# Optimization experiments

Hardware: AMD Instinct MI355X
Metric: run time of the kernel (lower is better)

The kernel has to match this reference:

```python
import jax, jax.numpy as jnp
import numpy as np

K = 10          # top-k history news selected per candidate
THRESHOLD = 0.1 # attention-weight threshold (config.threshold)
EPS = 1e-12     # F.normalize eps


def setup_inputs() -> dict:
    key = jax.random.key(0)
    k1, k2, k3, k4 = jax.random.split(key, 4)
    B, C, H, L, LEV, D = 32, 5, 50, 32, 3, 256
    return {
        "cdd_repr": jax.random.normal(k1, (B, C, D), dtype=jnp.float32),
        "his_repr": jax.random.normal(k2, (B, H, D), dtype=jnp.float32),
        "his_embedding": jax.random.normal(k3, (B, H, L, LEV, D), dtype=jnp.float32),
        "W_sel": jax.random.normal(k4, (D, D), dtype=jnp.float32) * (1.0 / np.sqrt(D)),
        "b_sel": jnp.zeros((D,), dtype=jnp.float32),
    }


def _l2norm(x):
    # F.normalize(x, dim=-1): x / max(||x||, eps)
    n = jnp.sqrt(jnp.sum(x * x, axis=-1, keepdims=True))
    return x / jnp.maximum(n, EPS)


def reference(cdd_repr, his_repr, his_embedding, W_sel, b_sel):
    # selectionProject (Linear) + L2 normalize
    c = _l2norm(cdd_repr @ W_sel + b_sel)      # [B, C, D]
    h = _l2norm(his_repr @ W_sel + b_sel)      # [B, H, D]
    # news-level attention scores: cdd x his
    attn = jnp.einsum('bcd,bhd->bch', c, h)    # [B, C, H]
    # top-k over history
    w, idx = jax.lax.top_k(attn, K)            # [B, C, K]
    # gather selected history embeddings: [B, C, K, L, LEV, D]
    B = his_embedding.shape[0]
    his_activated = his_embedding[jnp.arange(B)[:, None, None], idx]
    # threshold masking then scale activated embeddings by attention weight
    w_masked = jnp.where(w < THRESHOLD, 0.0, w)
    his_activated = his_activated * w_masked[:, :, :, None, None, None]
    return his_activated
```

## Files before the change

kernel.cpp:

```cpp
#include <hip/hip_runtime.h>
#include <math.h>

#define BB 32
#define CC 5
#define HH 50
#define LL 32
#define LEV 3
#define DD 256
#define KK 10
#define THRESH 0.1f
#define EPSF 1e-12f
#define RPB 8
#define NPROJ ((BB * CC + BB * HH) / RPB)
#define INNER (LL * LEV * DD)
#define INNER4 (INNER / 4)
#define NBCK (BB * CC * KK)
#define CHUNKS 4
#define PERCH (INNER4 / CHUNKS)

typedef float f32x4 __attribute__((ext_vector_type(4)));

__device__ __forceinline__ void store_stream(f32x4 v, f32x4* p) {
    asm volatile("global_store_dwordx4 %0, %1, off sc0 sc1 nt"
                 :: "v"(p), "v"(v) : "memory");
}

__global__ void proj_norm_kernel(const float* __restrict__ cdd,
                                 const float* __restrict__ his,
                                 const float* __restrict__ W,
                                 const float* __restrict__ bias,
                                 float* __restrict__ c_out,
                                 float* __restrict__ h_out)
{
    const int row0 = blockIdx.x * RPB;
    const int j    = threadIdx.x;
    const int wid  = j >> 6;
    const int lane = j & 63;

    __shared__ float xs[RPB][DD];
    #pragma unroll
    for (int r = 0; r < RPB; ++r) {
        const int row = row0 + r;
        const float* x = (row < BB * CC) ? (cdd + (size_t)row * DD)
                                         : (his + (size_t)(row - BB * CC) * DD);
        xs[r][j] = x[j];
    }
    __syncthreads();

    const float bj = bias[j];
    float acc[RPB];
    #pragma unroll
    for (int r = 0; r < RPB; ++r) acc[r] = bj;

    for (int d = 0; d < DD; d += 4) {
        const float w0 = W[(size_t)(d + 0) * DD + j];
        const float w1 = W[(size_t)(d + 1) * DD + j];
        const float w2 = W[(size_t)(d + 2) * DD + j];
        const float w3 = W[(size_t)(d + 3) * DD + j];
        #pragma unroll
        for (int r = 0; r < RPB; ++r) {
            const float4 xv = *(const float4*)&xs[r][d];
            acc[r] = fmaf(xv.x, w0, fmaf(xv.y, w1, fmaf(xv.z, w2, fmaf(xv.w, w3, acc[r]))));
        }
    }

    __shared__ float part[RPB][4];
    #pragma unroll
    for (int r = 0; r < RPB; ++r) {
        float s = acc[r] * acc[r];
        #pragma unroll
        for (int off = 32; off > 0; off >>= 1) s += __shfl_xor(s, off, 64);
        if (lane == 0) part[r][wid] = s;
    }
    __syncthreads();
    __shared__ float inv_s[RPB];
    if (j < RPB) {
        const float s = part[j][0] + part[j][1] + part[j][2] + part[j][3];
        inv_s[j] = 1.0f / fmaxf(sqrtf(s), EPSF);
    }
    __syncthreads();

    #pragma unroll
    for (int r = 0; r < RPB; ++r) {
        const int row = row0 + r;
        float* y = (row < BB * CC) ? (c_out + (size_t)row * DD)
                                   : (h_out + (size_t)(row - BB * CC) * DD);
        y[j] = acc[r] * inv_s[r];
    }
}

__global__ void attn_topk_kernel(const float* __restrict__ c_n,
                                 const float* __restrict__ h_n,
                                 float2* __restrict__ wvidx)
{
    const int bc   = blockIdx.x;
    const int b    = bc / CC;
    const int tid  = threadIdx.x;
    const int wid  = tid >> 6;
    const int lane = tid & 63;

    __shared__ float cs[DD];
    __shared__ float attn_s[64];
    cs[tid] = c_n[(size_t)bc * DD + tid];
    if (tid < 64) attn_s[tid] = -INFINITY;
    __syncthreads();

    for (int h = wid; h < HH; h += 4) {
        const float* hr = h_n + (size_t)(b * HH + h) * DD;
        float p = 0.f;
        #pragma unroll
        for (int i = 0; i < 4; ++i) p += cs[lane + i * 64] * hr[lane + i * 64];
        #pragma unroll
        for (int off = 32; off > 0; off >>= 1) p += __shfl_down(p, off, 64);
        if (lane == 0) attn_s[h] = p;
    }
    __syncthreads();

    if (wid == 0) {
        float v   = attn_s[lane];
        int   myi = lane;
        for (int k = 0; k < KK; ++k) {
            float bv = v;
            int   bi = myi;
            #pragma unroll
            for (int off = 32; off > 0; off >>= 1) {
                const float ov = __shfl_xor(bv, off, 64);
                const int   oi = __shfl_xor(bi, off, 64);
                if (ov > bv || (ov == bv && oi < bi)) { bv = ov; bi = oi; }
            }
            if (lane == 0)
                wvidx[bc * KK + k] = make_float2((bv < THRESH) ? 0.0f : bv,
                                                 __int_as_float(bi));
            if (myi == bi) v = -INFINITY;
        }
    }
}

__global__ __launch_bounds__(256)
void gather_scale_kernel(const float* __restrict__ emb,
                         const float2* __restrict__ wvidx,
                         float* __restrict__ out)
{
    const int g     = blockIdx.x;
    const int blk   = g >> 2;
    const int chunk = g & 3;
    const int b     = blk / (CC * KK);

    const float2 wi = wvidx[blk];
    const float  w_ = wi.x;

    f32x4* dst = (f32x4*)(out + (size_t)blk * INNER) + chunk * PERCH + threadIdx.x;

    if (w_ == 0.0f) {
        const f32x4 z = (f32x4){0.f, 0.f, 0.f, 0.f};
        #pragma unroll
        for (int u = 0; u < PERCH / 256; ++u)
            store_stream(z, dst + 256 * u);
    } else {
        const int hi = __float_as_int(wi.y);
        const f32x4* src = (const f32x4*)(emb + (size_t)(b * HH + hi) * INNER)
                           + chunk * PERCH + threadIdx.x;
        #pragma unroll
        for (int u = 0; u < PERCH / 256; ++u)
            store_stream(src[256 * u] * w_, dst + 256 * u);
    }
}

extern "C" void kernel_launch(void* const* d_in, const int* in_sizes, int n_in,
                              void* d_out, int out_size, void* d_ws, size_t ws_size,
                              hipStream_t stream) {
    const float* cdd  = (const float*)d_in[0];
    const float* his  = (const float*)d_in[1];
    const float* emb  = (const float*)d_in[2];
    const float* W    = (const float*)d_in[3];
    const float* bias = (const float*)d_in[4];
    float* out = (float*)d_out;

    char* ws = (char*)d_ws;
    float*  c_n   = (float*)ws;
    float*  h_n   = (float*)(ws + 163840);
    float2* wvidx = (float2*)(ws + 163840 + 1638400);

    proj_norm_kernel<<<NPROJ, DD, 0, stream>>>(cdd, his, W, bias, c_n, h_n);
    attn_topk_kernel<<<BB * CC, DD, 0, stream>>>(c_n, h_n, wvidx);
    gather_scale_kernel<<<NBCK * CHUNKS, 256, 0, stream>>>(emb, wvidx, out);
}
```

Before: 77.92 us.

## Fuse three kernels into one cooperative persistent kernel with grid syncs

Merges the projection/normalize, attention/top-k and gather-scale stages into a single cooperative kernel separated by grid-wide barriers. Blocks loop over work items in each stage. The aim is to remove two kernel launch gaps and their inter-kernel drain. In exchange it adds grid.sync overhead, per-call host queries of device attributes and occupancy, and a fixed grid size that may limit how well the memory-bound gather stage is parallelised.

```diff
diff --git a/kernel.cpp b/kernel.cpp
--- a/kernel.cpp
+++ b/kernel.cpp
@@ -1,5 +1,8 @@
 #include <hip/hip_runtime.h>
+#include <hip/hip_cooperative_groups.h>
 #include <math.h>
+
+namespace cg = cooperative_groups;
 
 #define BB 32
 #define CC 5
@@ -17,12 +20,158 @@
 #define NBCK (BB * CC * KK)
 #define CHUNKS 4
 #define PERCH (INNER4 / CHUNKS)
+#define NCHUNK (NBCK * CHUNKS)
 
 typedef float f32x4 __attribute__((ext_vector_type(4)));
 
 __device__ __forceinline__ void store_stream(f32x4 v, f32x4* p) {
     asm volatile("global_store_dwordx4 %0, %1, off sc0 sc1 nt"
                  :: "v"(p), "v"(v) : "memory");
+}
+
+__global__ __launch_bounds__(256)
+void fused_kernel(const float* __restrict__ cdd,
+                  const float* __restrict__ his,
+                  const float* __restrict__ emb,
+                  const float* __restrict__ W,
+                  const float* __restrict__ bias,
+                  float* __restrict__ c_n,
+                  float* __restrict__ h_n,
+                  float2* __restrict__ wvidx,
+                  float* __restrict__ out)
+{
+    cg::grid_group grid = cg::this_grid();
+    const int bid  = blockIdx.x;
+    const int nblk = gridDim.x;
+    const int j    = threadIdx.x;
+    const int wid  = j >> 6;
+    const int lane = j & 63;
+
+    __shared__ float xs[RPB][DD];
+    __shared__ float part[RPB][4];
+    __shared__ float inv_s[RPB];
+    __shared__ float cs[DD];
+    __shared__ float attn_s[64];
+
+    for (int pb = bid; pb < NPROJ; pb += nblk) {
+        const int row0 = pb * RPB;
+
+        #pragma unroll
+        for (int r = 0; r < RPB; ++r) {
+            const int row = row0 + r;
+            const float* x = (row < BB * CC) ? (cdd + (size_t)row * DD)
+                                             : (his + (size_t)(row - BB * CC) * DD);
+            xs[r][j] = x[j];
+        }
+        __syncthreads();
+
+        const float bj = bias[j];
+        float acc[RPB];
+        #pragma unroll
+        for (int r = 0; r < RPB; ++r) acc[r] = bj;
+
+        for (int d = 0; d < DD; d += 4) {
+            const float w0 = W[(size_t)(d + 0) * DD + j];
+            const float w1 = W[(size_t)(d + 1) * DD + j];
+            const float w2 = W[(size_t)(d + 2) * DD + j];
+            const float w3 = W[(size_t)(d + 3) * DD + j];
+            #pragma unroll
+            for (int r = 0; r < RPB; ++r) {
+                const float4 xv = *(const float4*)&xs[r][d];
+                acc[r] = fmaf(xv.x, w0, fmaf(xv.y, w1, fmaf(xv.z, w2, fmaf(xv.w, w3, acc[r]))));
+            }
+        }
+
+        #pragma unroll
+        for (int r = 0; r < RPB; ++r) {
+            float s = acc[r] * acc[r];
+            #pragma unroll
+            for (int off = 32; off > 0; off >>= 1) s += __shfl_xor(s, off, 64);
+            if (lane == 0) part[r][wid] = s;
+        }
+        __syncthreads();
+        if (j < RPB) {
+            const float s = part[j][0] + part[j][1] + part[j][2] + part[j][3];
+            inv_s[j] = 1.0f / fmaxf(sqrtf(s), EPSF);
+        }
+        __syncthreads();
+
+        #pragma unroll
+        for (int r = 0; r < RPB; ++r) {
+            const int row = row0 + r;
+            float* y = (row < BB * CC) ? (c_n + (size_t)row * DD)
+                                       : (h_n + (size_t)(row - BB * CC) * DD);
+            y[j] = acc[r] * inv_s[r];
+        }
+    }
+
+    grid.sync();
+
+    for (int bc = bid; bc < BB * CC; bc += nblk) {
+        const int b = bc / CC;
+
+        cs[j] = c_n[(size_t)bc * DD + j];
+        if (j < 64) attn_s[j] = -INFINITY;
+        __syncthreads();
+
+        for (int h = wid; h < HH; h += 4) {
+            const float* hr = h_n + (size_t)(b * HH + h) * DD;
+            float p = 0.f;
+            #pragma unroll
+            for (int i = 0; i < 4; ++i) p += cs[lane + i * 64] * hr[lane + i * 64];
+            #pragma unroll
+            for (int off = 32; off > 0; off >>= 1) p += __shfl_down(p, off, 64);
+            if (lane == 0) attn_s[h] = p;
+        }
+        __syncthreads();
+
+        if (wid == 0) {
+            float v   = attn_s[lane];
+            int   myi = lane;
+            for (int k = 0; k < KK; ++k) {
+                float bv = v;
+                int   bi = myi;
+                #pragma unroll
+                for (int off = 32; off > 0; off >>= 1) {
+                    const float ov = __shfl_xor(bv, off, 64);
+                    const int   oi = __shfl_xor(bi, off, 64);
+                    if (ov > bv || (ov == bv && oi < bi)) { bv = ov; bi = oi; }
+                }
+                if (lane == 0)
+                    wvidx[bc * KK + k] = make_float2((bv < THRESH) ? 0.0f : bv,
+                                                     __int_as_float(bi));
+                if (myi == bi) v = -INFINITY;
+            }
+        }
+        __syncthreads();
+    }
+
+    grid.sync();
+
+    for (int g = bid; g < NCHUNK; g += nblk) {
+        const int blk   = g >> 2;
+        const int chunk = g & 3;
+        const int b     = blk / (CC * KK);
+
+        const float2 wi = wvidx[blk];
+        const float  w_ = wi.x;
+
+        f32x4* dst = (f32x4*)(out + (size_t)blk * INNER) + chunk * PERCH + j;
+
+        if (w_ == 0.0f) {
+            const f32x4 z = (f32x4){0.f, 0.f, 0.f, 0.f};
+            #pragma unroll
+            for (int u = 0; u < PERCH / 256; ++u)
+                store_stream(z, dst + 256 * u);
+        } else {
+            const int hi = __float_as_int(wi.y);
+            const f32x4* src = (const f32x4*)(emb + (size_t)(b * HH + hi) * INNER)
+                               + chunk * PERCH + j;
+            #pragma unroll
+            for (int u = 0; u < PERCH / 256; ++u)
+                store_stream(src[256 * u] * w_, dst + 256 * u);
+        }
+    }
 }
 
 __global__ void proj_norm_kernel(const float* __restrict__ cdd,
@@ -181,7 +330,24 @@
     float*  h_n   = (float*)(ws + 163840);
     float2* wvidx = (float2*)(ws + 163840 + 1638400);
 
-    proj_norm_kernel<<<NPROJ, DD, 0, stream>>>(cdd, his, W, bias, c_n, h_n);
-    attn_topk_kernel<<<BB * CC, DD, 0, stream>>>(c_n, h_n, wvidx);
-    gather_scale_kernel<<<NBCK * CHUNKS, 256, 0, stream>>>(emb, wvidx, out);
-}
+    int dev = 0;
+    hipGetDevice(&dev);
+    int coop = 0, ncu = 0, maxbpc = 0;
+    hipDeviceGetAttribute(&coop, hipDeviceAttributeCooperativeLaunch, dev);
+    hipDeviceGetAttribute(&ncu, hipDeviceAttributeMultiprocessorCount, dev);
+    hipOccupancyMaxActiveBlocksPerMultiprocessor(&maxbpc, (const void*)fused_kernel, 256, 0);
+
+    long nblk = (long)maxbpc * (long)ncu;
+    if (nblk > NCHUNK) nblk = NCHUNK;
+
+    if (coop && nblk >= 512) {
+        void* args[] = { (void*)&cdd, (void*)&his, (void*)&emb, (void*)&W, (void*)&bias,
+                         (void*)&c_n, (void*)&h_n, (void*)&wvidx, (void*)&out };
+        hipLaunchCooperativeKernel((const void*)fused_kernel,
+                                   dim3((unsigned)nblk), dim3(256), args, 0, stream);
+    } else {
+        proj_norm_kernel<<<NPROJ, DD, 0, stream>>>(cdd, his, W, bias, c_n, h_n);
+        attn_topk_kernel<<<BB * CC, DD, 0, stream>>>(c_n, h_n, wvidx);
+        gather_scale_kernel<<<NCHUNK, 256, 0, stream>>>(emb, wvidx, out);
+    }
+}
```

Result: slower. 175.7 us (+125.5%).
